# Kernel tuning notes

Hardware: AMD Instinct MI355X
Metric: run time of the kernel (lower is better)

## Reference

```python
import jax, jax.numpy as jnp
import numpy as np

B, T = 32, 64
STOCH, DETER, HIDDEN = 1024, 4096, 1024
ACT_DIM, EMBED = 128, 1536
MIN_STD = 0.1
EPS = 1e-3  # dreamerv3-torch uses LayerNorm(eps=1e-3)


def _ln(x, g, b):
    m = jnp.mean(x, -1, keepdims=True)
    v = jnp.var(x, -1, keepdims=True)
    return (x - m) * jax.lax.rsqrt(v + EPS) * g + b


def setup_inputs() -> dict:
    key = jax.random.key(0)
    ks = jax.random.split(key, 24)

    def w(k, fan_in, fan_out):
        return jax.random.normal(k, (fan_in, fan_out), jnp.float32) / np.sqrt(fan_in)

    inp = {
        "embed": jax.random.normal(ks[0], (B, T, EMBED), jnp.float32),
        "action": jax.random.normal(ks[1], (B, T, ACT_DIM), jnp.float32),
        "is_first": jnp.zeros((B, T), jnp.bool_),
        "init_deter": jax.random.normal(ks[2], (B, DETER), jnp.float32),
        "init_stoch": jax.random.normal(ks[3], (B, STOCH), jnp.float32),
        "noise_prior": jax.random.normal(ks[4], (B, T, STOCH), jnp.float32),
        "noise_post": jax.random.normal(ks[5], (B, T, STOCH), jnp.float32),
        # _img_in_layers: Linear(stoch+act -> hidden, no bias) + LN + SiLU
        "W_in": w(ks[6], STOCH + ACT_DIM, HIDDEN),
        "g_in": 1.0 + 0.1 * jax.random.normal(ks[7], (HIDDEN,), jnp.float32),
        "b_in": 0.1 * jax.random.normal(ks[8], (HIDDEN,), jnp.float32),
        # GRUCell: Linear(hidden+deter -> 3*deter, no bias) + LN
        "W_gru": w(ks[9], HIDDEN + DETER, 3 * DETER),
        "g_gru": 1.0 + 0.1 * jax.random.normal(ks[10], (3 * DETER,), jnp.float32),
        "b_gru": 0.1 * jax.random.normal(ks[11], (3 * DETER,), jnp.float32),
        # _img_out_layers: Linear(deter -> hidden, no bias) + LN + SiLU
        "W_imgout": w(ks[12], DETER, HIDDEN),
        "g_io": 1.0 + 0.1 * jax.random.normal(ks[13], (HIDDEN,), jnp.float32),
        "b_io": 0.1 * jax.random.normal(ks[14], (HIDDEN,), jnp.float32),
        # _obs_out_layers: Linear(deter+embed -> hidden, no bias) + LN + SiLU
        "W_obsout": w(ks[15], DETER + EMBED, HIDDEN),
        "g_oo": 1.0 + 0.1 * jax.random.normal(ks[16], (HIDDEN,), jnp.float32),
        "b_oo": 0.1 * jax.random.normal(ks[17], (HIDDEN,), jnp.float32),
        # suff-stats layers: Linear(hidden -> 2*stoch) with bias
        "W_ims": w(ks[18], HIDDEN, 2 * STOCH),
        "b_ims": 0.01 * jax.random.normal(ks[19], (2 * STOCH,), jnp.float32),
        "W_obs": w(ks[20], HIDDEN, 2 * STOCH),
        "b_obs": 0.01 * jax.random.normal(ks[21], (2 * STOCH,), jnp.float32),
    }
    return inp


def _observe(embed, action, init_deter, init_stoch, noise_prior, noise_post,
             W_in, g_in, b_in, W_gru, g_gru, b_gru, W_imgout, g_io, b_io,
             W_obsout, g_oo, b_oo, W_ims, b_ims, W_obs, b_obs):
    def suff_stats(h, W, b, noise):
        stats = h @ W + b
        mean, std = jnp.split(stats, 2, -1)
        std = jax.nn.softplus(std) + MIN_STD  # std_act='softplus', mean_act='none'
        return mean, std, mean + std * noise

    def step(carry, xs):
        deter, stoch = carry
        e, a, n_p, n_q = xs
        # img_in: concat(prev_stoch, action) -> Linear -> LN -> SiLU
        x = jax.nn.silu(_ln(jnp.concatenate([stoch, a], -1) @ W_in, g_in, b_in))
        # GRUCell with layernorm (update_bias = -1)
        parts = _ln(jnp.concatenate([x, deter], -1) @ W_gru, g_gru, b_gru)
        reset, cand, update = jnp.split(parts, 3, -1)
        reset = jax.nn.sigmoid(reset)
        cand = jnp.tanh(reset * cand)
        update = jax.nn.sigmoid(update - 1.0)
        deter = update * cand + (1.0 - update) * deter
        # prior (imagination) suff stats + sample
        h_p = jax.nn.silu(_ln(deter @ W_imgout, g_io, b_io))
        mean_p, std_p, stoch_p = suff_stats(h_p, W_ims, b_ims, n_p)
        # posterior (observation) suff stats + sample
        h_q = jax.nn.silu(_ln(jnp.concatenate([deter, e], -1) @ W_obsout, g_oo, b_oo))
        mean_q, std_q, stoch_q = suff_stats(h_q, W_obs, b_obs, n_q)
        out = jnp.concatenate([deter, stoch_q, mean_q, std_q, stoch_p, mean_p, std_p], -1)
        return (deter, stoch_q), out

    xs = (jnp.swapaxes(embed, 0, 1), jnp.swapaxes(action, 0, 1),
          jnp.swapaxes(noise_prior, 0, 1), jnp.swapaxes(noise_post, 0, 1))
    _, outs = jax.lax.scan(step, (init_deter, init_stoch), xs)
    return jnp.swapaxes(outs, 0, 1)  # [B, T, deter + 6*stoch]


def reference(embed, action, is_first, init_deter, init_stoch, noise_prior, noise_post,
              W_in, g_in, b_in, W_gru, g_gru, b_gru, W_imgout, g_io, b_io,
              W_obsout, g_oo, b_oo, W_ims, b_ims, W_obs, b_obs):
    # is_first is all-False and state is given, so the init-mixing branch is never taken
    del is_first
    return _observe(embed, action, init_deter, init_stoch, noise_prior, noise_post,
                    W_in, g_in, b_in, W_gru, g_gru, b_gru, W_imgout, g_io, b_io,
                    W_obsout, g_oo, b_oo, W_ims, b_ims, W_obs, b_obs)
```

## Files before the change

### kernel.cpp

```cpp
#include <hip/hip_runtime.h>
#include <hip/hip_bf16.h>

#define T_ 64
#define DETER_ 4096
#define GRUN 12288

typedef __attribute__((ext_vector_type(8))) __bf16 bf16x8;
typedef __attribute__((ext_vector_type(4))) float f32x4;
typedef __attribute__((ext_vector_type(8))) unsigned short u16x8;
typedef __attribute__((ext_vector_type(4))) unsigned short u16x4;

__device__ inline unsigned short f2bf(float f) {
    union { float f; unsigned u; } x; x.f = f;
    unsigned r = x.u + 0x7fffu + ((x.u >> 16) & 1u);
    return (unsigned short)(r >> 16);
}
__device__ inline float sigmoidf_(float v) { return 1.f / (1.f + __expf(-v)); }
__device__ inline float siluf_(float v)    { return v / (1.f + __expf(-v)); }
__device__ inline float softplusf_(float v){ return fmaxf(v, 0.f) + __logf(1.f + __expf(-fabsf(v))); }
__device__ inline float tanhf_(float v)    { return 2.f / (1.f + __expf(-2.f * v)) - 1.f; }

__device__ inline void barrier_() {
    asm volatile("" ::: "memory");
    __builtin_amdgcn_s_barrier();
    asm volatile("" ::: "memory");
}
template <int N> __device__ inline void vmwaitN() {
    asm volatile("s_waitcnt vmcnt(%0)" :: "i"(N) : "memory");
}
__device__ inline void lgkmwait_() {
    asm volatile("s_waitcnt lgkmcnt(0)" ::: "memory");
}


__global__ __launch_bounds__(256) void k_pack(const float* __restrict__ W,
                                              unsigned short* __restrict__ dst,
                                              int K, int N) {
    long fid = (long)blockIdx.x * 256 + threadIdx.x;
    long nfr = (long)K * N / 8;
    if (fid >= nfr) return;
    int lane = (int)(fid & 63);
    long tile = fid >> 6;
    int ktiles = K >> 5;
    int k_t = (int)(tile % ktiles);
    int n_t = (int)(tile / ktiles);
    int c = lane & 15, kb = lane >> 4;
    int k0 = k_t * 32 + kb * 8;
    int n = n_t * 16 + c;
    unsigned short v[8];
#pragma unroll
    for (int i = 0; i < 8; i++) v[i] = f2bf(W[(long)(k0 + i) * N + n]);
    *reinterpret_cast<u16x8*>(dst + fid * 8) = *reinterpret_cast<u16x8*>(v);
}

__global__ __launch_bounds__(256) void k_conv(const float* __restrict__ s,
                                              unsigned short* __restrict__ d, long n) {
    long i = ((long)blockIdx.x * 256 + threadIdx.x) * 4;
    if (i >= n) return;
    f32x4 v = *reinterpret_cast<const f32x4*>(s + i);
    unsigned short o[4];
#pragma unroll
    for (int k = 0; k < 4; k++) o[k] = f2bf(v[k]);
    *reinterpret_cast<u16x4*>(d + i) = *reinterpret_cast<u16x4*>(o);
}

__global__ __launch_bounds__(256) void k_copy(const float* __restrict__ s,
                                              float* __restrict__ d, long n) {
    long i = ((long)blockIdx.x * 256 + threadIdx.x) * 4;
    if (i >= n) return;
    *reinterpret_cast<f32x4*>(d + i) = *reinterpret_cast<const f32x4*>(s + i);
}


template <int CW>
__device__ inline void stage_glds(unsigned short* chunk, const unsigned short* __restrict__ src,
                                  long ld, long k0) {
    constexpr int NI = (32 * CW * 2) / 4096;
    int wv = (int)threadIdx.x >> 6, lane = (int)threadIdx.x & 63;
#pragma unroll
    for (int i = 0; i < NI; ++i) {
        int obase = (wv * NI + i) << 10;
        int o = obase + lane * 16;
        int row = o / (CW * 2);
        int cb = o - row * (CW * 2);
        int gb = cb ^ ((row & 7) << 4);
        const char* ga = (const char*)(src + (long)row * ld + k0) + gb;
        __builtin_amdgcn_global_load_lds(
            (const __attribute__((address_space(1))) void*)ga,
            (__attribute__((address_space(3))) void*)(chunk + (obase >> 1)),
            16, 0, 0);
    }
}

__device__ inline void stage_ln512(unsigned short* chunk, const float* __restrict__ raw,
                                   int ld, int col0,
                                   const float* __restrict__ g, const float* __restrict__ b,
                                   const float* s_mean, const float* s_rstd) {
    int tid = threadIdx.x;
#pragma unroll
    for (int i = 0; i < 8; ++i) {
        int e = tid * 8 + i * 2048;
        int row = e >> 9, col = e & 511;
        float m = s_mean[row], rs = s_rstd[row];
        const float* sp = raw + (long)row * ld + col0 + col;
        unsigned short pk[8];
#pragma unroll
        for (int j = 0; j < 8; ++j) {
            float ln = (sp[j] - m) * rs * g[col0 + col + j] + b[col0 + col + j];
            pk[j] = f2bf(siluf_(ln));
        }
        int dcol = col ^ ((row & 7) << 3);
        *reinterpret_cast<u16x8*>(chunk + row * 512 + dcol) = *reinterpret_cast<u16x8*>(pk);
    }
}

__device__ inline void stage_lnsum(unsigned short* chunk, const float* __restrict__ hpart,
                                   const float* __restrict__ eprep, int t, int col0,
                                   const float* __restrict__ g, const float* __restrict__ b,
                                   const float* s_mean, const float* s_rstd) {
    int tid = threadIdx.x;
#pragma unroll
    for (int i = 0; i < 8; ++i) {
        int e = tid * 8 + i * 2048;
        int row = e >> 9, col = e & 511;
        int k = col0 + col;
        float m = s_mean[row], rs = s_rstd[row];
        const float* h0 = hpart + (long)row * 1024 + k;
        const float* ep = eprep + ((long)row * T_ + t) * 1024 + k;
        unsigned short pk[8];
#pragma unroll
        for (int jj = 0; jj < 8; jj += 4) {
            f32x4 v = *reinterpret_cast<const f32x4*>(h0 + jj);
            v += *reinterpret_cast<const f32x4*>(h0 + 32768 + jj);
            v += *reinterpret_cast<const f32x4*>(h0 + 65536 + jj);
            v += *reinterpret_cast<const f32x4*>(h0 + 98304 + jj);
            v += *reinterpret_cast<const f32x4*>(ep + jj);
#pragma unroll
            for (int j2 = 0; j2 < 4; ++j2) {
                float ln = (v[j2] - m) * rs * g[k + jj + j2] + b[k + jj + j2];
                pk[jj + j2] = f2bf(siluf_(ln));
            }
        }
        int dcol = col ^ ((row & 7) << 3);
        *reinterpret_cast<u16x8*>(chunk + row * 512 + dcol) = *reinterpret_cast<u16x8*>(pk);
    }
}

template <int CW>
__device__ inline void mfma_rh(const unsigned short* chunk, int row, int kb,
                               const unsigned short* __restrict__ bp, f32x4& acc) {
    constexpr int NKT = CW / 32;
    const unsigned short* ap = chunk + row * CW;
    int sw = (row & 7) << 3;
#pragma unroll
    for (int kt = 0; kt < NKT; ++kt) {
        bf16x8 a = *reinterpret_cast<const bf16x8*>(ap + ((kb * 8 + kt * 32) ^ sw));
        bf16x8 b = *reinterpret_cast<const bf16x8*>(bp + (long)kt * 512);
        acc = __builtin_amdgcn_mfma_f32_16x16x32_bf16(a, b, acc, 0, 0, 0);
    }
}

template <int CW>
__device__ inline void mfma2(const unsigned short* chunk, int c, int kb,
                             const unsigned short* __restrict__ bp,
                             f32x4& acc0, f32x4& acc1) {
    constexpr int NKT = CW / 32;
    const unsigned short* ap0 = chunk + c * CW;
    const unsigned short* ap1 = chunk + (16 + c) * CW;
    int sw = (c & 7) << 3;
#pragma unroll
    for (int kt = 0; kt < NKT; ++kt) {
        int off = (kb * 8 + kt * 32) ^ sw;
        bf16x8 b = *reinterpret_cast<const bf16x8*>(bp + (long)kt * 512);
        bf16x8 a0 = *reinterpret_cast<const bf16x8*>(ap0 + off);
        bf16x8 a1 = *reinterpret_cast<const bf16x8*>(ap1 + off);
        acc0 = __builtin_amdgcn_mfma_f32_16x16x32_bf16(a0, b, acc0, 0, 0, 0);
        acc1 = __builtin_amdgcn_mfma_f32_16x16x32_bf16(a1, b, acc1, 0, 0, 0);
    }
}

template <int CW, int NG, int NL>
__global__ __launch_bounds__(256) void k_gemm32(
    const unsigned short* __restrict__ Bp, int Ktiles, int ktg0,
    const unsigned short* __restrict__ srcA, long ldA,
    const float* __restrict__ lnraw, int lnld,
    const float* __restrict__ g_ln, const float* __restrict__ b_ln,
    const float* __restrict__ pstats, int nslab_in,
    const float* __restrict__ addin, long addin_ld,
    float* __restrict__ outp, long out_ld,
    float* __restrict__ partials, long prows)
{
    constexpr int NCH = NG + NL;
    constexpr int NI = (32 * CW * 2) / 4096;
    __shared__ __align__(16) unsigned short sb[2][32 * CW];
    __shared__ float s_out[32][34];
    __shared__ float s_mean[32], s_rstd[32];
    int tid = threadIdx.x;
    if (NL > 0) {
        if (tid < 32) {
            float s = 0.f, q = 0.f;
            for (int j = 0; j < nslab_in; ++j) {
                s += pstats[((long)j * 32 + tid) * 2];
                q += pstats[((long)j * 32 + tid) * 2 + 1];
            }
            float m = s * (1.f / 1024.f);
            s_mean[tid] = m;
            s_rstd[tid] = rsqrtf(q * (1.f / 1024.f) - m * m + 1e-3f);
        }
        __syncthreads();
    }
    int rowbase = blockIdx.y * 32;
    const unsigned short* srcAr = srcA + (long)rowbase * ldA;
    int lane = tid & 63, wv = tid >> 6;
    int nt = wv >> 1, rh = wv & 1;
    int c = lane & 15, kb = lane >> 4;
    int mrow = rh * 16 + c;
    long ntg = (long)blockIdx.x * 2 + nt;
    const unsigned short* bbase = Bp + (long)ntg * Ktiles * 512 + lane * 8;
    f32x4 acc = {0.f, 0.f, 0.f, 0.f};
    stage_glds<CW>(sb[0], srcAr, ldA, 0);
    for (int ch = 0; ch < NCH; ++ch) {
        int nx = ch + 1;
        if (nx < NG) stage_glds<CW>(sb[nx & 1], srcAr, ldA, (long)nx * CW);
        else if (nx < NCH) stage_ln512(sb[nx & 1], lnraw, lnld, (nx - NG) * 512,
                                       g_ln, b_ln, s_mean, s_rstd);
        if (ch < NG) { if (nx < NG) vmwaitN<NI>(); else vmwaitN<0>(); }
        if (nx >= NG && nx < NCH) lgkmwait_();
        barrier_();
        int kt0 = (ch < NG) ? (ktg0 + ch * (CW / 32)) : ((ch - NG) * 16);
        mfma_rh<CW>(sb[ch & 1], mrow, kb, bbase + (long)kt0 * 512, acc);
        barrier_();
    }
    __syncthreads();
#pragma unroll
    for (int j = 0; j < 4; ++j) s_out[rh * 16 + kb * 4 + j][nt * 16 + c] = acc[j];
    __syncthreads();
    int orow = tid >> 3, c4 = (tid & 7) * 4;
    long rg = rowbase + orow;
    float v[4]; float s = 0.f, q = 0.f;
#pragma unroll
    for (int i = 0; i < 4; ++i) {
        float x = s_out[orow][c4 + i];
        if (addin) x += addin[rg * addin_ld + blockIdx.x * 32 + c4 + i];
        v[i] = x; s += x; q += x * x;
    }
#pragma unroll
    for (int i = 0; i < 4; ++i) outp[rg * out_ld + blockIdx.x * 32 + c4 + i] = v[i];
    if (partials) {
#pragma unroll
        for (int m = 1; m < 8; m <<= 1) { s += __shfl_xor(s, m); q += __shfl_xor(q, m); }
        if ((tid & 7) == 0) {
            partials[((long)blockIdx.x * prows + rg) * 2] = s;
            partials[((long)blockIdx.x * prows + rg) * 2 + 1] = q;
        }
    }
}

__global__ __launch_bounds__(256) void k_gru2(
    const unsigned short* __restrict__ Bp,
    const unsigned short* __restrict__ deterb,
    const float* __restrict__ x_raw, const float* __restrict__ px,
    const float* __restrict__ g_in, const float* __restrict__ b_in,
    float* __restrict__ Gp0, float* __restrict__ Gp1)
{
    __shared__ __align__(16) unsigned short sb[2][32 * 512];
    __shared__ float s_out[32][66];
    __shared__ float s_mean[32], s_rstd[32];
    int tid = threadIdx.x, lane = tid & 63, wv = tid >> 6;
    int c = lane & 15, kb = lane >> 4;
    long ntg = (long)blockIdx.x * 4 + wv;
    const unsigned short* bbase = Bp + ntg * 160 * 512 + lane * 8;
    f32x4 acc0 = {0,0,0,0}, acc1 = {0,0,0,0};

    if (blockIdx.y == 0) {
        if (tid < 32) {
            float s = 0.f, q = 0.f;
            for (int j = 0; j < 32; ++j) {
                s += px[((long)j * 32 + tid) * 2];
                q += px[((long)j * 32 + tid) * 2 + 1];
            }
            float m = s * (1.f / 1024.f);
            s_mean[tid] = m;
            s_rstd[tid] = rsqrtf(q * (1.f / 1024.f) - m * m + 1e-3f);
        }
        __syncthreads();
        stage_glds<512>(sb[0], deterb, 4096, 0);
        stage_glds<512>(sb[1], deterb, 4096, 512);
        vmwaitN<8>(); barrier_();
        mfma2<512>(sb[0], c, kb, bbase + 32 * 512, acc0, acc1);
        barrier_();
        stage_glds<512>(sb[0], deterb, 4096, 1024);
        vmwaitN<8>(); barrier_();
        mfma2<512>(sb[1], c, kb, bbase + 48 * 512, acc0, acc1);
        barrier_();
        stage_ln512(sb[1], x_raw, 1024, 0, g_in, b_in, s_mean, s_rstd);
        vmwaitN<0>(); barrier_();
        mfma2<512>(sb[0], c, kb, bbase + 64 * 512, acc0, acc1);
        barrier_();
        stage_ln512(sb[0], x_raw, 1024, 512, g_in, b_in, s_mean, s_rstd);
        lgkmwait_(); barrier_();
        mfma2<512>(sb[1], c, kb, bbase + 0, acc0, acc1);
        barrier_();
        mfma2<512>(sb[0], c, kb, bbase + 16 * 512, acc0, acc1);
    } else {
        stage_glds<512>(sb[0], deterb, 4096, 1536);
        stage_glds<512>(sb[1], deterb, 4096, 2048);
        vmwaitN<8>(); barrier_();
        mfma2<512>(sb[0], c, kb, bbase + 80 * 512, acc0, acc1);
        barrier_();
        stage_glds<512>(sb[0], deterb, 4096, 2560);
        vmwaitN<8>(); barrier_();
        mfma2<512>(sb[1], c, kb, bbase + 96 * 512, acc0, acc1);
        barrier_();
        stage_glds<512>(sb[1], deterb, 4096, 3072);
        vmwaitN<8>(); barrier_();
        mfma2<512>(sb[0], c, kb, bbase + 112 * 512, acc0, acc1);
        barrier_();
        stage_glds<512>(sb[0], deterb, 4096, 3584);
        vmwaitN<8>(); barrier_();
        mfma2<512>(sb[1], c, kb, bbase + 128 * 512, acc0, acc1);
        barrier_();
        vmwaitN<0>(); barrier_();
        mfma2<512>(sb[0], c, kb, bbase + 144 * 512, acc0, acc1);
    }
    __syncthreads();
#pragma unroll
    for (int j = 0; j < 4; ++j) {
        s_out[kb * 4 + j][wv * 16 + c] = acc0[j];
        s_out[16 + kb * 4 + j][wv * 16 + c] = acc1[j];
    }
    __syncthreads();
    float* G = (blockIdx.y == 0) ? Gp0 : Gp1;
    int row = tid >> 3, c8 = (tid & 7) * 8;
#pragma unroll
    for (int i = 0; i < 8; ++i)
        G[(long)row * GRUN + blockIdx.x * 64 + c8 + i] = s_out[row][c8 + i];
}

__global__ __launch_bounds__(1024) void k_deter2(
    const float* __restrict__ Gp0, const float* __restrict__ Gp1,
    const float* __restrict__ g_gru, const float* __restrict__ b_gru,
    float* __restrict__ deterf, unsigned short* __restrict__ deterb,
    unsigned short* __restrict__ deter_allb, float* __restrict__ out, int t)
{
    __shared__ float gsh[GRUN];
    __shared__ float red[32];
    int r = blockIdx.x, tid = threadIdx.x;
    int lane = tid & 63, wv = tid >> 6;
    const float* a0 = Gp0 + (long)r * GRUN;
    const float* a1 = Gp1 + (long)r * GRUN;
    float s = 0.f, q = 0.f;
#pragma unroll
    for (int i = 0; i < 3; ++i) {
        int col = (tid + i * 1024) * 4;
        f32x4 v = *reinterpret_cast<const f32x4*>(a0 + col);
        v += *reinterpret_cast<const f32x4*>(a1 + col);
        *reinterpret_cast<f32x4*>(gsh + col) = v;
#pragma unroll
        for (int j = 0; j < 4; ++j) { s += v[j]; q += v[j] * v[j]; }
    }
#pragma unroll
    for (int m = 1; m < 64; m <<= 1) { s += __shfl_xor(s, m); q += __shfl_xor(q, m); }
    if (lane == 0) { red[wv] = s; red[16 + wv] = q; }
    __syncthreads();
    float fs = 0.f, fq = 0.f;
#pragma unroll
    for (int i = 0; i < 16; ++i) { fs += red[i]; fq += red[16 + i]; }
    float mean = fs * (1.f / 12288.f);
    float rstd = rsqrtf(fq * (1.f / 12288.f) - mean * mean + 1e-3f);
    long orow = (long)r * T_ + t;
#pragma unroll
    for (int it = 0; it < 2; ++it) {
        int j = tid * 2 + it * 2048;
        float2 rr = *reinterpret_cast<const float2*>(gsh + j);
        float2 cc = *reinterpret_cast<const float2*>(gsh + 4096 + j);
        float2 uu = *reinterpret_cast<const float2*>(gsh + 8192 + j);
        float2 dd = *reinterpret_cast<const float2*>(deterf + (long)r * DETER_ + j);
        float dn[2]; unsigned short db[2];
#pragma unroll
        for (int i = 0; i < 2; ++i) {
            float gv = (i == 0) ? rr.x : rr.y;
            float cv = (i == 0) ? cc.x : cc.y;
            float uv = (i == 0) ? uu.x : uu.y;
            float dv = (i == 0) ? dd.x : dd.y;
            float lr = (gv - mean) * rstd * g_gru[j + i] + b_gru[j + i];
            float lc = (cv - mean) * rstd * g_gru[4096 + j + i] + b_gru[4096 + j + i];
            float lu = (uv - mean) * rstd * g_gru[8192 + j + i] + b_gru[8192 + j + i];
            float reset = sigmoidf_(lr);
            float cand = tanhf_(reset * lc);
            float upd = sigmoidf_(lu - 1.f);
            dn[i] = upd * cand + (1.f - upd) * dv;
            db[i] = f2bf(dn[i]);
        }
        float2 nd; nd.x = dn[0]; nd.y = dn[1];
        *reinterpret_cast<float2*>(deterf + (long)r * DETER_ + j) = nd;
        unsigned pk = (unsigned)db[0] | ((unsigned)db[1] << 16);
        *reinterpret_cast<unsigned*>(deterb + (long)r * DETER_ + j) = pk;
        *reinterpret_cast<unsigned*>(deter_allb + orow * DETER_ + j) = pk;
        *reinterpret_cast<float2*>(out + orow * 10240 + j) = nd;
    }
}

__global__ __launch_bounds__(256) void k_h4(
    const unsigned short* __restrict__ Wood,
    const unsigned short* __restrict__ deterb,
    float* __restrict__ hpart)
{
    __shared__ __align__(16) unsigned short sb[2][32 * 512];
    __shared__ float s_out[32][66];
    int tid = threadIdx.x, lane = tid & 63, wv = tid >> 6;
    int c = lane & 15, kb = lane >> 4;
    int n = blockIdx.x, kq = blockIdx.y;
    const unsigned short* bbase = Wood + ((long)(n * 4 + wv) * 128) * 512 + lane * 8;
    f32x4 acc0 = {0,0,0,0}, acc1 = {0,0,0,0};
    stage_glds<512>(sb[0], deterb, 4096, (long)kq * 1024);
    stage_glds<512>(sb[1], deterb, 4096, (long)kq * 1024 + 512);
    vmwaitN<8>(); barrier_();
    mfma2<512>(sb[0], c, kb, bbase + (long)(kq * 32) * 512, acc0, acc1);
    vmwaitN<0>(); barrier_();
    mfma2<512>(sb[1], c, kb, bbase + (long)(kq * 32 + 16) * 512, acc0, acc1);
    __syncthreads();
#pragma unroll
    for (int j = 0; j < 4; ++j) {
        s_out[kb * 4 + j][wv * 16 + c] = acc0[j];
        s_out[16 + kb * 4 + j][wv * 16 + c] = acc1[j];
    }
    __syncthreads();
    int row = tid >> 3, c8 = (tid & 7) * 8;
    float* hp = hpart + (long)kq * 32768 + (long)row * 1024 + n * 64 + c8;
#pragma unroll
    for (int i = 0; i < 8; ++i) hp[i] = s_out[row][c8 + i];
}

__global__ __launch_bounds__(256) void k_statsq2(
    const unsigned short* __restrict__ Bp, const float* __restrict__ hpart,
    const float* __restrict__ E_pre,
    const float* __restrict__ g_oo, const float* __restrict__ b_oo,
    const float* __restrict__ bias,
    const float* __restrict__ noise, float* __restrict__ out,
    unsigned short* __restrict__ stochb, int t)
{
    __shared__ __align__(16) unsigned short sb[2][32 * 512];
    __shared__ float s_out[32][66];
    __shared__ float s_mean[32], s_rstd[32];
    int tid = threadIdx.x, lane = tid & 63, wv = tid >> 6;
    int c = lane & 15, kb = lane >> 4;
    {
        int row = tid >> 3, c0 = (tid & 7) * 128;
        const float* h0 = hpart + (long)row * 1024 + c0;
        const float* ep = E_pre + ((long)row * T_ + t) * 1024 + c0;
        float s = 0.f, q = 0.f;
#pragma unroll 8
        for (int kk = 0; kk < 128; kk += 4) {
            f32x4 v = *reinterpret_cast<const f32x4*>(h0 + kk);
            v += *reinterpret_cast<const f32x4*>(h0 + 32768 + kk);
            v += *reinterpret_cast<const f32x4*>(h0 + 65536 + kk);
            v += *reinterpret_cast<const f32x4*>(h0 + 98304 + kk);
            v += *reinterpret_cast<const f32x4*>(ep + kk);
#pragma unroll
            for (int j2 = 0; j2 < 4; ++j2) { s += v[j2]; q += v[j2] * v[j2]; }
        }
#pragma unroll
        for (int m = 1; m < 8; m <<= 1) { s += __shfl_xor(s, m); q += __shfl_xor(q, m); }
        if ((tid & 7) == 0) {
            float mm = s * (1.f / 1024.f);
            s_mean[row] = mm;
            s_rstd[row] = rsqrtf(q * (1.f / 1024.f) - mm * mm + 1e-3f);
        }
    }
    __syncthreads();
    int part = wv >> 1, nt = wv & 1;
    long ntg = (long)part * 64 + blockIdx.x * 2 + nt;
    const unsigned short* bbase = Bp + ntg * 32 * 512 + lane * 8;
    f32x4 acc0 = {0,0,0,0}, acc1 = {0,0,0,0};
    stage_lnsum(sb[0], hpart, E_pre, t, 0, g_oo, b_oo, s_mean, s_rstd);
    stage_lnsum(sb[1], hpart, E_pre, t, 512, g_oo, b_oo, s_mean, s_rstd);
    lgkmwait_(); barrier_();
    mfma2<512>(sb[0], c, kb, bbase, acc0, acc1);
    mfma2<512>(sb[1], c, kb, bbase + 16 * 512, acc0, acc1);
    __syncthreads();
    float bv = bias[ntg * 16 + c];
#pragma unroll
    for (int j = 0; j < 4; ++j) {
        s_out[kb * 4 + j][part * 32 + nt * 16 + c] = acc0[j] + bv;
        s_out[16 + kb * 4 + j][part * 32 + nt * 16 + c] = acc1[j] + bv;
    }
    __syncthreads();
    int r = tid >> 3, j0 = (tid & 7) * 4;
    long orow = (long)r * T_ + t;
#pragma unroll
    for (int i = 0; i < 4; ++i) {
        int j = j0 + i;
        float mean = s_out[r][j];
        float sd = softplusf_(s_out[r][32 + j]) + 0.1f;
        int cg2 = blockIdx.x * 32 + j;
        float st = mean + sd * noise[orow * 1024 + cg2];
        float* op = out + orow * 10240;
        op[4096 + cg2] = st; op[5120 + cg2] = mean; op[6144 + cg2] = sd;
        stochb[(long)r * 1024 + cg2] = f2bf(st);
    }
}

__global__ __launch_bounds__(256) void k_bstats(
    const unsigned short* __restrict__ Bp, const unsigned short* __restrict__ h_pb,
    const float* __restrict__ bias, const float* __restrict__ noise,
    float* __restrict__ out)
{
    __shared__ __align__(16) unsigned short sb[2][32 * 512];
    __shared__ float s_out[32][66];
    int tid = threadIdx.x;
    int lane = tid & 63, wv = tid >> 6;
    int part = wv >> 1, nt = wv & 1;
    int c = lane & 15, kb = lane >> 4;
    int s_ = blockIdx.x, rowbase = blockIdx.y * 32;
    const unsigned short* A = h_pb + (long)rowbase * 1024;
    long ntg = (long)part * 64 + s_ * 2 + nt;
    const unsigned short* bbase = Bp + ntg * 32 * 512 + lane * 8;
    f32x4 acc0 = {0.f,0.f,0.f,0.f}, acc1 = {0.f,0.f,0.f,0.f};
    stage_glds<512>(sb[0], A, 1024, 0);
    stage_glds<512>(sb[1], A, 1024, 512);
    vmwaitN<8>(); barrier_();
    mfma_rh<512>(sb[0], c, kb, bbase, acc0);
    mfma_rh<512>(sb[0], 16 + c, kb, bbase, acc1);
    vmwaitN<0>(); barrier_();
    mfma_rh<512>(sb[1], c, kb, bbase + 16 * 512, acc0);
    mfma_rh<512>(sb[1], 16 + c, kb, bbase + 16 * 512, acc1);
    __syncthreads();
    float bv = bias[ntg * 16 + c];
#pragma unroll
    for (int j = 0; j < 4; ++j) {
        s_out[kb * 4 + j][part * 32 + nt * 16 + c] = acc0[j] + bv;
        s_out[16 + kb * 4 + j][part * 32 + nt * 16 + c] = acc1[j] + bv;
    }
    __syncthreads();
    int r = tid >> 3, j0 = (tid & 7) * 4;
    long orow = rowbase + r;
#pragma unroll
    for (int i = 0; i < 4; ++i) {
        int j = j0 + i;
        float mean = s_out[r][j];
        float sd = softplusf_(s_out[r][32 + j]) + 0.1f;
        int cg2 = s_ * 32 + j;
        float st = mean + sd * noise[orow * 1024 + cg2];
        float* op = out + orow * 10240;
        op[7168 + cg2] = st; op[8192 + cg2] = mean; op[9216 + cg2] = sd;
    }
}

__global__ __launch_bounds__(256) void k_bfin(const float* __restrict__ hp_raw,
                                              const float* __restrict__ pbh,
                                              const float* __restrict__ g_io,
                                              const float* __restrict__ b_io,
                                              unsigned short* __restrict__ h_pb) {
    int row = blockIdx.x * 8 + ((int)threadIdx.x >> 5);
    int l = threadIdx.x & 31;
    float s = pbh[((long)l * 2048 + row) * 2];
    float q = pbh[((long)l * 2048 + row) * 2 + 1];
#pragma unroll
    for (int m = 16; m; m >>= 1) { s += __shfl_xor(s, m, 32); q += __shfl_xor(q, m, 32); }
    float mn = s * (1.f / 1024.f);
    float rs = rsqrtf(q * (1.f / 1024.f) - mn * mn + 1e-3f);
#pragma unroll
    for (int i = 0; i < 8; ++i) {
        int col = i * 128 + l * 4;
        f32x4 v = *reinterpret_cast<const f32x4*>(hp_raw + (long)row * 1024 + col);
        unsigned short pk[4];
#pragma unroll
        for (int j = 0; j < 4; ++j) {
            float ln = (v[j] - mn) * rs * g_io[col + j] + b_io[col + j];
            pk[j] = f2bf(siluf_(ln));
        }
        *reinterpret_cast<u16x4*>(h_pb + (long)row * 1024 + col) = *reinterpret_cast<u16x4*>(pk);
    }
}


extern "C" void kernel_launch(void* const* d_in, const int* in_sizes, int n_in,
                              void* d_out, int out_size, void* d_ws, size_t ws_size,
                              hipStream_t stream) {
    const float* embed      = (const float*)d_in[0];
    const float* action     = (const float*)d_in[1];
    const float* init_deter = (const float*)d_in[3];
    const float* init_stoch = (const float*)d_in[4];
    const float* noise_pr   = (const float*)d_in[5];
    const float* noise_po   = (const float*)d_in[6];
    const float* W_in       = (const float*)d_in[7];
    const float* g_in       = (const float*)d_in[8];
    const float* b_in       = (const float*)d_in[9];
    const float* W_gru      = (const float*)d_in[10];
    const float* g_gru      = (const float*)d_in[11];
    const float* b_gru      = (const float*)d_in[12];
    const float* W_io       = (const float*)d_in[13];
    const float* g_io       = (const float*)d_in[14];
    const float* b_io       = (const float*)d_in[15];
    const float* W_oo       = (const float*)d_in[16];
    const float* g_oo       = (const float*)d_in[17];
    const float* b_oo       = (const float*)d_in[18];
    const float* W_ims      = (const float*)d_in[19];
    const float* b_ims      = (const float*)d_in[20];
    const float* W_obs      = (const float*)d_in[21];
    const float* b_obs      = (const float*)d_in[22];
    float* out = (float*)d_out;

    char* ws = (char*)d_ws;
    size_t off = 0;
    auto alloc = [&](size_t bytes) {
        size_t r = off;
        off = (off + bytes + 255) & ~(size_t)255;
        return r;
    };
    unsigned short* pWgru  = (unsigned short*)(ws + alloc((size_t)5120 * 12288 * 2));
    unsigned short* pWin_s = (unsigned short*)(ws + alloc((size_t)1024 * 1024 * 2));
    unsigned short* pWin_a = (unsigned short*)(ws + alloc((size_t)128 * 1024 * 2));
    unsigned short* pWio   = (unsigned short*)(ws + alloc((size_t)4096 * 1024 * 2));
    unsigned short* pWood  = (unsigned short*)(ws + alloc((size_t)4096 * 1024 * 2));
    unsigned short* pWooe  = (unsigned short*)(ws + alloc((size_t)1536 * 1024 * 2));
    unsigned short* pWims  = (unsigned short*)(ws + alloc((size_t)1024 * 2048 * 2));
    unsigned short* pWobs  = (unsigned short*)(ws + alloc((size_t)1024 * 2048 * 2));
    unsigned short* act_bf = (unsigned short*)(ws + alloc((size_t)2048 * 128 * 2));
    unsigned short* emb_bf = (unsigned short*)(ws + alloc((size_t)2048 * 1536 * 2));
    float* A_pre  = (float*)(ws + alloc((size_t)2048 * 1024 * 4));
    float* E_pre  = (float*)(ws + alloc((size_t)2048 * 1024 * 4));
    float* x_raw  = (float*)(ws + alloc((size_t)32 * 1024 * 4));
    float* Gp0    = (float*)(ws + alloc((size_t)32 * GRUN * 4));
    float* Gp1    = (float*)(ws + alloc((size_t)32 * GRUN * 4));
    float* deterf = (float*)(ws + alloc((size_t)32 * DETER_ * 4));
    unsigned short* deterb     = (unsigned short*)(ws + alloc((size_t)32 * DETER_ * 2));
    unsigned short* deter_allb = (unsigned short*)(ws + alloc((size_t)2048 * DETER_ * 2));
    unsigned short* stochb = (unsigned short*)(ws + alloc((size_t)32 * 1024 * 2));
    float* hp_raw = (float*)(ws + alloc((size_t)2048 * 1024 * 4));
    unsigned short* h_pb = (unsigned short*)(ws + alloc((size_t)2048 * 1024 * 2));
    float* px  = (float*)(ws + alloc((size_t)32 * 32 * 2 * 4));
    float* pbh = (float*)(ws + alloc((size_t)32 * 2048 * 2 * 4));
    float* hpart = (float*)(ws + alloc((size_t)4 * 32 * 1024 * 4));
    (void)ws_size; (void)out_size; (void)n_in; (void)in_sizes;

    auto packgrid = [](long K, long N) { return (unsigned)((K * N / 8 + 255) / 256); };

    k_pack<<<packgrid(5120, 12288), 256, 0, stream>>>(W_gru, pWgru, 5120, 12288);
    k_pack<<<packgrid(1024, 1024), 256, 0, stream>>>(W_in, pWin_s, 1024, 1024);
    k_pack<<<packgrid(128, 1024), 256, 0, stream>>>(W_in + (size_t)1024 * 1024, pWin_a, 128, 1024);
    k_pack<<<packgrid(4096, 1024), 256, 0, stream>>>(W_io, pWio, 4096, 1024);
    k_pack<<<packgrid(4096, 1024), 256, 0, stream>>>(W_oo, pWood, 4096, 1024);
    k_pack<<<packgrid(1536, 1024), 256, 0, stream>>>(W_oo + (size_t)4096 * 1024, pWooe, 1536, 1024);
    k_pack<<<packgrid(1024, 2048), 256, 0, stream>>>(W_ims, pWims, 1024, 2048);
    k_pack<<<packgrid(1024, 2048), 256, 0, stream>>>(W_obs, pWobs, 1024, 2048);
    k_conv<<<(2048 * 128 / 4 + 255) / 256, 256, 0, stream>>>(action, act_bf, 2048L * 128);
    k_conv<<<(2048 * 1536 / 4 + 255) / 256, 256, 0, stream>>>(embed, emb_bf, 2048L * 1536);
    k_conv<<<(32 * 1024 / 4 + 255) / 256, 256, 0, stream>>>(init_stoch, stochb, 32L * 1024);
    k_conv<<<(32 * 4096 / 4 + 255) / 256, 256, 0, stream>>>(init_deter, deterb, 32L * 4096);
    k_copy<<<(32 * 4096 / 4 + 255) / 256, 256, 0, stream>>>(init_deter, deterf, 32L * 4096);
    k_gemm32<128, 1, 0><<<dim3(32, 64), 256, 0, stream>>>(
        pWin_a, 4, 0, act_bf, 128, nullptr, 0, nullptr, nullptr, nullptr, 0,
        nullptr, 0, A_pre, 1024, nullptr, 0);
    k_gemm32<512, 3, 0><<<dim3(32, 64), 256, 0, stream>>>(
        pWooe, 48, 0, emb_bf, 1536, nullptr, 0, nullptr, nullptr, nullptr, 0,
        nullptr, 0, E_pre, 1024, nullptr, 0);

    for (int t = 0; t < T_; ++t) {
        k_gemm32<512, 2, 0><<<dim3(32, 1), 256, 0, stream>>>(
            pWin_s, 32, 0, stochb, 1024, nullptr, 0, nullptr, nullptr, nullptr, 0,
            A_pre + (size_t)t * 1024, (long)T_ * 1024, x_raw, 1024, px, 32);
        k_gru2<<<dim3(192, 2), 256, 0, stream>>>(pWgru, deterb, x_raw, px, g_in, b_in,
                                                 Gp0, Gp1);
        k_deter2<<<32, 1024, 0, stream>>>(Gp0, Gp1, g_gru, b_gru, deterf, deterb,
                                          deter_allb, out, t);
        k_h4<<<dim3(16, 4), 256, 0, stream>>>(pWood, deterb, hpart);
        k_statsq2<<<32, 256, 0, stream>>>(pWobs, hpart, E_pre, g_oo, b_oo, b_obs,
                                          noise_po, out, stochb, t);
    }

    k_gemm32<512, 8, 0><<<dim3(32, 64), 256, 0, stream>>>(
        pWio, 128, 0, deter_allb, 4096, nullptr, 0, nullptr, nullptr, nullptr, 0,
        nullptr, 0, hp_raw, 1024, pbh, 2048);
    k_bfin<<<256, 256, 0, stream>>>(hp_raw, pbh, g_io, b_io, h_pb);
    k_bstats<<<dim3(32, 64), 256, 0, stream>>>(pWims, h_pb, b_ims, noise_pr, out);
}
```

Measured before the change: 7.000 ms.

## Split GRU and obs-out GEMMs into more K-slices with register-prefetched weights

The per-step GRU GEMM now splits K four ways instead of two (grid 192x4), and the obs-out hidden GEMM splits eight ways instead of four (grid 16x8). Both raise parallelism for the small-batch, latency-bound recurrence. Weight fragments are loaded into registers up front (loadB16) so those global loads overlap the LDS staging. The statsq kernel issues its weight loads before the LayerNorm reduction. In exchange, the consumer kernels read and sum more fp32 partial buffers, and register pressure rises from holding 32 bf16x8 weight fragments per lane.

```diff
diff --git a/kernel.cpp b/kernel.cpp
--- a/kernel.cpp
+++ b/kernel.cpp
@@ -31,6 +31,7 @@
 __device__ inline void lgkmwait_() {
     asm volatile("s_waitcnt lgkmcnt(0)" ::: "memory");
 }
+__device__ inline void cfence_() { asm volatile("" ::: "memory"); }
 
 
 __global__ __launch_bounds__(256) void k_pack(const float* __restrict__ W,
@@ -114,10 +115,19 @@
     }
 }
 
-__device__ inline void stage_lnsum(unsigned short* chunk, const float* __restrict__ hpart,
-                                   const float* __restrict__ eprep, int t, int col0,
-                                   const float* __restrict__ g, const float* __restrict__ b,
-                                   const float* s_mean, const float* s_rstd) {
+__device__ inline f32x4 hsum8(const float* __restrict__ h0, const float* __restrict__ ep, int off) {
+    f32x4 v = *reinterpret_cast<const f32x4*>(h0 + off);
+#pragma unroll
+    for (int q = 1; q < 8; ++q)
+        v += *reinterpret_cast<const f32x4*>(h0 + q * 32768 + off);
+    v += *reinterpret_cast<const f32x4*>(ep + off);
+    return v;
+}
+
+__device__ inline void stage_lnsum8(unsigned short* chunk, const float* __restrict__ hpart,
+                                    const float* __restrict__ eprep, int t, int col0,
+                                    const float* __restrict__ g, const float* __restrict__ b,
+                                    const float* s_mean, const float* s_rstd) {
     int tid = threadIdx.x;
 #pragma unroll
     for (int i = 0; i < 8; ++i) {
@@ -130,11 +140,7 @@
         unsigned short pk[8];
 #pragma unroll
         for (int jj = 0; jj < 8; jj += 4) {
-            f32x4 v = *reinterpret_cast<const f32x4*>(h0 + jj);
-            v += *reinterpret_cast<const f32x4*>(h0 + 32768 + jj);
-            v += *reinterpret_cast<const f32x4*>(h0 + 65536 + jj);
-            v += *reinterpret_cast<const f32x4*>(h0 + 98304 + jj);
-            v += *reinterpret_cast<const f32x4*>(ep + jj);
+            f32x4 v = hsum8(h0, ep, jj);
 #pragma unroll
             for (int j2 = 0; j2 < 4; ++j2) {
                 float ln = (v[j2] - m) * rs * g[k + jj + j2] + b[k + jj + j2];
@@ -176,6 +182,27 @@
         bf16x8 a1 = *reinterpret_cast<const bf16x8*>(ap1 + off);
         acc0 = __builtin_amdgcn_mfma_f32_16x16x32_bf16(a0, b, acc0, 0, 0, 0);
         acc1 = __builtin_amdgcn_mfma_f32_16x16x32_bf16(a1, b, acc1, 0, 0, 0);
+    }
+}
+
+__device__ inline void loadB16(bf16x8* br, const unsigned short* __restrict__ bp) {
+#pragma unroll
+    for (int kt = 0; kt < 16; ++kt)
+        br[kt] = *reinterpret_cast<const bf16x8*>(bp + (long)kt * 512);
+}
+
+__device__ inline void mfma2r(const unsigned short* chunk, int c, int kb,
+                              const bf16x8* br, f32x4& acc0, f32x4& acc1) {
+    const unsigned short* ap0 = chunk + c * 512;
+    const unsigned short* ap1 = chunk + (16 + c) * 512;
+    int sw = (c & 7) << 3;
+#pragma unroll
+    for (int kt = 0; kt < 16; ++kt) {
+        int off = (kb * 8 + kt * 32) ^ sw;
+        bf16x8 a0 = *reinterpret_cast<const bf16x8*>(ap0 + off);
+        bf16x8 a1 = *reinterpret_cast<const bf16x8*>(ap1 + off);
+        acc0 = __builtin_amdgcn_mfma_f32_16x16x32_bf16(a0, br[kt], acc0, 0, 0, 0);
+        acc1 = __builtin_amdgcn_mfma_f32_16x16x32_bf16(a1, br[kt], acc1, 0, 0, 0);
     }
 }
 
@@ -256,23 +283,25 @@
     }
 }
 
-__global__ __launch_bounds__(256) void k_gru2(
+__global__ __launch_bounds__(256, 2) void k_gru4(
     const unsigned short* __restrict__ Bp,
     const unsigned short* __restrict__ deterb,
     const float* __restrict__ x_raw, const float* __restrict__ px,
     const float* __restrict__ g_in, const float* __restrict__ b_in,
-    float* __restrict__ Gp0, float* __restrict__ Gp1)
+    float* __restrict__ Gp)
 {
     __shared__ __align__(16) unsigned short sb[2][32 * 512];
     __shared__ float s_out[32][66];
     __shared__ float s_mean[32], s_rstd[32];
     int tid = threadIdx.x, lane = tid & 63, wv = tid >> 6;
     int c = lane & 15, kb = lane >> 4;
+    int kq = blockIdx.y;
     long ntg = (long)blockIdx.x * 4 + wv;
-    const unsigned short* bbase = Bp + ntg * 160 * 512 + lane * 8;
-    f32x4 acc0 = {0,0,0,0}, acc1 = {0,0,0,0};
-
-    if (blockIdx.y == 0) {
+    const unsigned short* bb = Bp + ntg * 160 * 512 + lane * 8;
+    f32x4 acc0 = {0, 0, 0, 0}, acc1 = {0, 0, 0, 0};
+    bf16x8 br0[16], br1[16];
+
+    if (kq == 0) {
         if (tid < 32) {
             float s = 0.f, q = 0.f;
             for (int j = 0; j < 32; ++j) {
@@ -284,44 +313,46 @@
             s_rstd[tid] = rsqrtf(q * (1.f / 1024.f) - m * m + 1e-3f);
         }
         __syncthreads();
-        stage_glds<512>(sb[0], deterb, 4096, 0);
-        stage_glds<512>(sb[1], deterb, 4096, 512);
-        vmwaitN<8>(); barrier_();
-        mfma2<512>(sb[0], c, kb, bbase + 32 * 512, acc0, acc1);
+        loadB16(br0, bb);
+        loadB16(br1, bb + 16 * 512);
+        stage_ln512(sb[0], x_raw, 1024, 0, g_in, b_in, s_mean, s_rstd);
+        stage_ln512(sb[1], x_raw, 1024, 512, g_in, b_in, s_mean, s_rstd);
+        lgkmwait_(); barrier_();
+        mfma2r(sb[0], c, kb, br0, acc0, acc1);
+        mfma2r(sb[1], c, kb, br1, acc0, acc1);
+    } else {
+        int nch = (kq == 3) ? 2 : 3;
+        long o0 = (long)(kq - 1) * 1536;
+        int t0 = 32 + (kq - 1) * 48;
+        stage_glds<512>(sb[0], deterb, 4096, o0);
+        cfence_();
+        loadB16(br0, bb + (long)t0 * 512);
+        cfence_();
+        stage_glds<512>(sb[1], deterb, 4096, o0 + 512);
+        cfence_();
+        loadB16(br1, bb + (long)(t0 + 16) * 512);
+        cfence_();
+        vmwaitN<24>();
         barrier_();
-        stage_glds<512>(sb[0], deterb, 4096, 1024);
-        vmwaitN<8>(); barrier_();
-        mfma2<512>(sb[1], c, kb, bbase + 48 * 512, acc0, acc1);
+        mfma2r(sb[0], c, kb, br0, acc0, acc1);
         barrier_();
-        stage_ln512(sb[1], x_raw, 1024, 0, g_in, b_in, s_mean, s_rstd);
-        vmwaitN<0>(); barrier_();
-        mfma2<512>(sb[0], c, kb, bbase + 64 * 512, acc0, acc1);
-        barrier_();
-        stage_ln512(sb[0], x_raw, 1024, 512, g_in, b_in, s_mean, s_rstd);
-        lgkmwait_(); barrier_();
-        mfma2<512>(sb[1], c, kb, bbase + 0, acc0, acc1);
-        barrier_();
-        mfma2<512>(sb[0], c, kb, bbase + 16 * 512, acc0, acc1);
-    } else {
-        stage_glds<512>(sb[0], deterb, 4096, 1536);
-        stage_glds<512>(sb[1], deterb, 4096, 2048);
-        vmwaitN<8>(); barrier_();
-        mfma2<512>(sb[0], c, kb, bbase + 80 * 512, acc0, acc1);
-        barrier_();
-        stage_glds<512>(sb[0], deterb, 4096, 2560);
-        vmwaitN<8>(); barrier_();
-        mfma2<512>(sb[1], c, kb, bbase + 96 * 512, acc0, acc1);
-        barrier_();
-        stage_glds<512>(sb[1], deterb, 4096, 3072);
-        vmwaitN<8>(); barrier_();
-        mfma2<512>(sb[0], c, kb, bbase + 112 * 512, acc0, acc1);
-        barrier_();
-        stage_glds<512>(sb[0], deterb, 4096, 3584);
-        vmwaitN<8>(); barrier_();
-        mfma2<512>(sb[1], c, kb, bbase + 128 * 512, acc0, acc1);
-        barrier_();
-        vmwaitN<0>(); barrier_();
-        mfma2<512>(sb[0], c, kb, bbase + 144 * 512, acc0, acc1);
+        if (nch == 3) {
+            stage_glds<512>(sb[0], deterb, 4096, o0 + 1024);
+            cfence_();
+            loadB16(br0, bb + (long)(t0 + 32) * 512);
+            cfence_();
+            vmwaitN<24>();
+            barrier_();
+            mfma2r(sb[1], c, kb, br1, acc0, acc1);
+            barrier_();
+            vmwaitN<0>();
+            barrier_();
+            mfma2r(sb[0], c, kb, br0, acc0, acc1);
+        } else {
+            vmwaitN<0>();
+            barrier_();
+            mfma2r(sb[1], c, kb, br1, acc0, acc1);
+        }
     }
     __syncthreads();
 #pragma unroll
@@ -330,15 +361,14 @@
         s_out[16 + kb * 4 + j][wv * 16 + c] = acc1[j];
     }
     __syncthreads();
-    float* G = (blockIdx.y == 0) ? Gp0 : Gp1;
     int row = tid >> 3, c8 = (tid & 7) * 8;
-#pragma unroll
-    for (int i = 0; i < 8; ++i)
-        G[(long)row * GRUN + blockIdx.x * 64 + c8 + i] = s_out[row][c8 + i];
-}
-
-__global__ __launch_bounds__(1024) void k_deter2(
-    const float* __restrict__ Gp0, const float* __restrict__ Gp1,
+    float* G = Gp + (long)kq * 32 * GRUN + (long)row * GRUN + blockIdx.x * 64 + c8;
+#pragma unroll
+    for (int i = 0; i < 8; ++i) G[i] = s_out[row][c8 + i];
+}
+
+__global__ __launch_bounds__(1024) void k_deter4(
+    const float* __restrict__ Gp,
     const float* __restrict__ g_gru, const float* __restrict__ b_gru,
     float* __restrict__ deterf, unsigned short* __restrict__ deterb,
     unsigned short* __restrict__ deter_allb, float* __restrict__ out, int t)
@@ -347,14 +377,15 @@
     __shared__ float red[32];
     int r = blockIdx.x, tid = threadIdx.x;
     int lane = tid & 63, wv = tid >> 6;
-    const float* a0 = Gp0 + (long)r * GRUN;
-    const float* a1 = Gp1 + (long)r * GRUN;
+    const float* g0 = Gp + (long)r * GRUN;
     float s = 0.f, q = 0.f;
 #pragma unroll
     for (int i = 0; i < 3; ++i) {
         int col = (tid + i * 1024) * 4;
-        f32x4 v = *reinterpret_cast<const f32x4*>(a0 + col);
-        v += *reinterpret_cast<const f32x4*>(a1 + col);
+        f32x4 v = *reinterpret_cast<const f32x4*>(g0 + col);
+        v += *reinterpret_cast<const f32x4*>(g0 + 393216 + col);
+        v += *reinterpret_cast<const f32x4*>(g0 + 786432 + col);
+        v += *reinterpret_cast<const f32x4*>(g0 + 1179648 + col);
         *reinterpret_cast<f32x4*>(gsh + col) = v;
 #pragma unroll
         for (int j = 0; j < 4; ++j) { s += v[j]; q += v[j] * v[j]; }
@@ -401,24 +432,26 @@
     }
 }
 
-__global__ __launch_bounds__(256) void k_h4(
+__global__ __launch_bounds__(256, 2) void k_h8(
     const unsigned short* __restrict__ Wood,
     const unsigned short* __restrict__ deterb,
     float* __restrict__ hpart)
 {
-    __shared__ __align__(16) unsigned short sb[2][32 * 512];
+    __shared__ __align__(16) unsigned short sb[32 * 512];
     __shared__ float s_out[32][66];
     int tid = threadIdx.x, lane = tid & 63, wv = tid >> 6;
     int c = lane & 15, kb = lane >> 4;
     int n = blockIdx.x, kq = blockIdx.y;
-    const unsigned short* bbase = Wood + ((long)(n * 4 + wv) * 128) * 512 + lane * 8;
-    f32x4 acc0 = {0,0,0,0}, acc1 = {0,0,0,0};
-    stage_glds<512>(sb[0], deterb, 4096, (long)kq * 1024);
-    stage_glds<512>(sb[1], deterb, 4096, (long)kq * 1024 + 512);
-    vmwaitN<8>(); barrier_();
-    mfma2<512>(sb[0], c, kb, bbase + (long)(kq * 32) * 512, acc0, acc1);
-    vmwaitN<0>(); barrier_();
-    mfma2<512>(sb[1], c, kb, bbase + (long)(kq * 32 + 16) * 512, acc0, acc1);
+    const unsigned short* bb = Wood + ((long)(n * 4 + wv) * 128 + kq * 16) * 512 + lane * 8;
+    f32x4 acc0 = {0, 0, 0, 0}, acc1 = {0, 0, 0, 0};
+    bf16x8 br[16];
+    stage_glds<512>(sb, deterb, 4096, (long)kq * 512);
+    cfence_();
+    loadB16(br, bb);
+    cfence_();
+    vmwaitN<0>();
+    barrier_();
+    mfma2r(sb, c, kb, br, acc0, acc1);
     __syncthreads();
 #pragma unroll
     for (int j = 0; j < 4; ++j) {
@@ -432,7 +465,7 @@
     for (int i = 0; i < 8; ++i) hp[i] = s_out[row][c8 + i];
 }
 
-__global__ __launch_bounds__(256) void k_statsq2(
+__global__ __launch_bounds__(256) void k_statsq8(
     const unsigned short* __restrict__ Bp, const float* __restrict__ hpart,
     const float* __restrict__ E_pre,
     const float* __restrict__ g_oo, const float* __restrict__ b_oo,
@@ -445,6 +478,12 @@
     __shared__ float s_mean[32], s_rstd[32];
     int tid = threadIdx.x, lane = tid & 63, wv = tid >> 6;
     int c = lane & 15, kb = lane >> 4;
+    int part = wv >> 1, nt = wv & 1;
+    long ntg = (long)part * 64 + blockIdx.x * 2 + nt;
+    const unsigned short* bb = Bp + ntg * 32 * 512 + lane * 8;
+    bf16x8 br0[16], br1[16];
+    loadB16(br0, bb);
+    loadB16(br1, bb + 16 * 512);
     {
         int row = tid >> 3, c0 = (tid & 7) * 128;
         const float* h0 = hpart + (long)row * 1024 + c0;
@@ -452,11 +491,7 @@
         float s = 0.f, q = 0.f;
 #pragma unroll 8
         for (int kk = 0; kk < 128; kk += 4) {
-            f32x4 v = *reinterpret_cast<const f32x4*>(h0 + kk);
-            v += *reinterpret_cast<const f32x4*>(h0 + 32768 + kk);
-            v += *reinterpret_cast<const f32x4*>(h0 + 65536 + kk);
-            v += *reinterpret_cast<const f32x4*>(h0 + 98304 + kk);
-            v += *reinterpret_cast<const f32x4*>(ep + kk);
+            f32x4 v = hsum8(h0, ep, kk);
 #pragma unroll
             for (int j2 = 0; j2 < 4; ++j2) { s += v[j2]; q += v[j2] * v[j2]; }
         }
@@ -469,15 +504,12 @@
         }
     }
     __syncthreads();
-    int part = wv >> 1, nt = wv & 1;
-    long ntg = (long)part * 64 + blockIdx.x * 2 + nt;
-    const unsigned short* bbase = Bp + ntg * 32 * 512 + lane * 8;
-    f32x4 acc0 = {0,0,0,0}, acc1 = {0,0,0,0};
-    stage_lnsum(sb[0], hpart, E_pre, t, 0, g_oo, b_oo, s_mean, s_rstd);
-    stage_lnsum(sb[1], hpart, E_pre, t, 512, g_oo, b_oo, s_mean, s_rstd);
+    f32x4 acc0 = {0, 0, 0, 0}, acc1 = {0, 0, 0, 0};
+    stage_lnsum8(sb[0], hpart, E_pre, t, 0, g_oo, b_oo, s_mean, s_rstd);
+    stage_lnsum8(sb[1], hpart, E_pre, t, 512, g_oo, b_oo, s_mean, s_rstd);
     lgkmwait_(); barrier_();
-    mfma2<512>(sb[0], c, kb, bbase, acc0, acc1);
-    mfma2<512>(sb[1], c, kb, bbase + 16 * 512, acc0, acc1);
+    mfma2r(sb[0], c, kb, br0, acc0, acc1);
+    mfma2r(sb[1], c, kb, br1, acc0, acc1);
     __syncthreads();
     float bv = bias[ntg * 16 + c];
 #pragma unroll
@@ -622,8 +654,7 @@
     float* A_pre  = (float*)(ws + alloc((size_t)2048 * 1024 * 4));
     float* E_pre  = (float*)(ws + alloc((size_t)2048 * 1024 * 4));
     float* x_raw  = (float*)(ws + alloc((size_t)32 * 1024 * 4));
-    float* Gp0    = (float*)(ws + alloc((size_t)32 * GRUN * 4));
-    float* Gp1    = (float*)(ws + alloc((size_t)32 * GRUN * 4));
+    float* Gp     = (float*)(ws + alloc((size_t)4 * 32 * GRUN * 4));
     float* deterf = (float*)(ws + alloc((size_t)32 * DETER_ * 4));
     unsigned short* deterb     = (unsigned short*)(ws + alloc((size_t)32 * DETER_ * 2));
     unsigned short* deter_allb = (unsigned short*)(ws + alloc((size_t)2048 * DETER_ * 2));
@@ -632,7 +663,7 @@
     unsigned short* h_pb = (unsigned short*)(ws + alloc((size_t)2048 * 1024 * 2));
     float* px  = (float*)(ws + alloc((size_t)32 * 32 * 2 * 4));
     float* pbh = (float*)(ws + alloc((size_t)32 * 2048 * 2 * 4));
-    float* hpart = (float*)(ws + alloc((size_t)4 * 32 * 1024 * 4));
+    float* hpart = (float*)(ws + alloc((size_t)8 * 32 * 1024 * 4));
     (void)ws_size; (void)out_size; (void)n_in; (void)in_sizes;
 
     auto packgrid = [](long K, long N) { return (unsigned)((K * N / 8 + 255) / 256); };
@@ -661,12 +692,11 @@
         k_gemm32<512, 2, 0><<<dim3(32, 1), 256, 0, stream>>>(
             pWin_s, 32, 0, stochb, 1024, nullptr, 0, nullptr, nullptr, nullptr, 0,
             A_pre + (size_t)t * 1024, (long)T_ * 1024, x_raw, 1024, px, 32);
-        k_gru2<<<dim3(192, 2), 256, 0, stream>>>(pWgru, deterb, x_raw, px, g_in, b_in,
-                                                 Gp0, Gp1);
-        k_deter2<<<32, 1024, 0, stream>>>(Gp0, Gp1, g_gru, b_gru, deterf, deterb,
+        k_gru4<<<dim3(192, 4), 256, 0, stream>>>(pWgru, deterb, x_raw, px, g_in, b_in, Gp);
+        k_deter4<<<32, 1024, 0, stream>>>(Gp, g_gru, b_gru, deterf, deterb,
                                           deter_allb, out, t);
-        k_h4<<<dim3(16, 4), 256, 0, stream>>>(pWood, deterb, hpart);
-        k_statsq2<<<32, 256, 0, stream>>>(pWobs, hpart, E_pre, g_oo, b_oo, b_obs,
+        k_h8<<<dim3(16, 8), 256, 0, stream>>>(pWood, deterb, hpart);
+        k_statsq8<<<32, 256, 0, stream>>>(pWobs, hpart, E_pre, g_oo, b_oo, b_obs,
                                           noise_po, out, stochb, t);
     }
 
```

Measured after the change: 8.202 ms. +17.2%, slower.
